# Performance work log

Hardware: AMD Instinct MI355X
Metric: run time of the kernel (lower is better)

The kernel has to match this reference:

```python
import jax, jax.numpy as jnp
import numpy as np

DIM = 1024
TOPK = 64
PAIRS = DIM // 2  # phase_pairs default
PHASE_MIX = 0.5
GATE_THRESHOLD = 0.0
EPS = 1e-12  # F.normalize default eps


def _l2norm(v):
    # matches F.normalize(v, dim=-1): v / max(||v||, eps)
    n = jnp.linalg.norm(v, axis=-1, keepdims=True)
    return v / jnp.maximum(n, EPS)


def setup_inputs() -> dict:
    key = jax.random.key(0)
    ks = jax.random.split(key, 6)
    s = 0.02  # small init scale for weights
    return {
        "x": jax.random.normal(ks[0], (4, 4096, DIM), dtype=jnp.float32),
        "gate_W": jax.random.normal(ks[1], (DIM, DIM), dtype=jnp.float32) * s,
        "gate_b": jnp.zeros((DIM,), dtype=jnp.float32),
        "mag_W": jax.random.normal(ks[2], (DIM, DIM), dtype=jnp.float32) * s,
        "mag_b": jnp.zeros((DIM,), dtype=jnp.float32),
        "Wq": jax.random.normal(ks[3], (DIM, DIM), dtype=jnp.float32) * s,
        "Wk": jax.random.normal(ks[4], (DIM, DIM), dtype=jnp.float32) * s,
        "phase_W": jax.random.normal(ks[5], (2 * PAIRS, DIM), dtype=jnp.float32) * s,
    }


def reference(x, gate_W, gate_b, mag_W, mag_b, Wq, Wk, phase_W):
    B, S, D = x.shape
    # gated SAE-style projection (gated=True, diag=False)
    gate_pre = x @ gate_W.T + gate_b          # [B,S,D]
    mag_pre = x @ mag_W.T + mag_b             # [B,S,D]
    # hard gate with straight-through estimator
    gate_soft = jax.nn.sigmoid(gate_pre)
    gate_hard = (gate_pre > GATE_THRESHOLD).astype(x.dtype)
    gate = gate_hard + gate_soft - jax.lax.stop_gradient(gate_soft)
    mag = jax.nn.relu(mag_pre)
    # top-k scatter mask along feature dim
    idx = jax.lax.top_k(gate_pre, TOPK)[1]    # [B,S,K]
    rows = jnp.arange(B * S)[:, None]
    mask = (jnp.zeros((B * S, D), dtype=bool)
            .at[rows, idx.reshape(B * S, TOPK)].set(True)
            .reshape(B, S, D))
    gate = jnp.where(mask, gate, jnp.zeros_like(gate))
    mag = jnp.where(mask, mag, jnp.zeros_like(mag))
    xg = gate * mag
    # twist projections, L2-normalized
    q = _l2norm(xg @ Wq.T)
    k = _l2norm(xg @ Wk.T)
    # symplectic momentum map over consecutive steps
    momentum_map = q[:, 1:] * k[:, :-1] - q[:, :-1] * k[:, 1:]  # [B,S-1,D]
    twist_mag = jnp.linalg.norm(momentum_map, axis=-1, keepdims=True)
    complexity = jnp.pad(jnp.tanh(twist_mag), ((0, 0), (1, 0), (0, 0)))  # [B,S,1]
    # phase branch (phase_mix > 0)
    phase = (xg @ phase_W.T).reshape(B, S, PAIRS, 2)
    phase = _l2norm(phase)
    pp, pc = phase[:, :-1], phase[:, 1:]
    cross = pp[..., 0] * pc[..., 1] - pp[..., 1] * pc[..., 0]   # [B,S-1,P]
    dot = jnp.clip(jnp.sum(pp * pc, axis=-1), -1.0, 1.0)
    phase_delta = jnp.abs(jnp.arctan2(cross, dot)) / jnp.pi
    phase_score = jnp.pad(jnp.mean(phase_delta, axis=-1, keepdims=True),
                          ((0, 0), (1, 0), (0, 0)))             # [B,S,1]
    return (1.0 - PHASE_MIX) * complexity + PHASE_MIX * phase_score
```

## Files before the change

kernel.cpp:

```cpp
#include <hip/hip_runtime.h>
#include <math.h>

#define DIM 1024
#define ROWS 16384
#define SEQ 4096
#define MARGIN 0.012f
#define MAXC 24

typedef __bf16 v8bf __attribute__((ext_vector_type(8)));
typedef float v4f __attribute__((ext_vector_type(4)));
typedef int v8i __attribute__((ext_vector_type(8)));

__device__ __forceinline__ unsigned short f2bf(float f){
  unsigned u = __float_as_uint(f);
  u = u + 0x7FFFu + ((u >> 16) & 1u);
  return (unsigned short)(u >> 16);
}
__device__ __forceinline__ float bf2f(unsigned short h){
  return __uint_as_float(((unsigned)h) << 16);
}
__device__ __forceinline__ unsigned short relu_bf(unsigned short h){
  return (h & 0x8000u) ? (unsigned short)0 : h;
}
__device__ __forceinline__ unsigned f2fp8(float f){
  float a = fabsf(f);
  unsigned sign = (__float_as_uint(f) >> 24) & 0x80u;
  if (a >= 448.f) return sign | 0x7Eu;
  if (a < 0.015625f){
    int k = (int)rintf(a * 512.f);
    if (k >= 8) return sign | 0x08u;
    return sign | (unsigned)k;
  }
  unsigned u = __float_as_uint(a);
  u += 0x7FFFFu + ((u >> 20) & 1u);
  int e = (int)((u >> 23) & 0xFFu) - 127;
  unsigned m = (u >> 20) & 7u;
  if (e > 8) return sign | 0x7Eu;
  return sign | ((unsigned)(e + 7) << 3) | m;
}
__device__ __forceinline__ void lds_fence(){
  __asm__ volatile("s_waitcnt lgkmcnt(0)" ::: "memory");
}

__global__ __launch_bounds__(256) void cvt_all(
    const float* __restrict__ x,
    const float* __restrict__ w0, const float* __restrict__ w1,
    const float* __restrict__ w2, const float* __restrict__ w3,
    const float* __restrict__ w4,
    unsigned short* __restrict__ xbf, unsigned short* __restrict__ wbf,
    unsigned char* __restrict__ wf8){
  const int y = blockIdx.y;
  int i = (blockIdx.x * 256 + threadIdx.x) * 4;
  if (y < 16){
    const float* s = x + ((size_t)y << 20);
    float4 f = *(const float4*)(s + i);
    ushort4 o; o.x = f2bf(f.x); o.y = f2bf(f.y); o.z = f2bf(f.z); o.w = f2bf(f.w);
    *(ushort4*)(xbf + ((size_t)y << 20) + i) = o;
  } else if (y < 18){
    const float* s = (y == 16) ? w0 : w1;
    float4 f = *(const float4*)(s + i);
    ushort4 o; o.x = f2bf(f.x); o.y = f2bf(f.y); o.z = f2bf(f.z); o.w = f2bf(f.w);
    *(ushort4*)(wbf + ((size_t)(y - 16) << 20) + i) = o;
  } else {
    const float* s = (y == 18) ? w2 : ((y == 19) ? w3 : w4);
    float4 f = *(const float4*)(s + i);
    unsigned u = f2fp8(f.x * 32.f) | (f2fp8(f.y * 32.f) << 8) |
                 (f2fp8(f.z * 32.f) << 16) | (f2fp8(f.w * 32.f) << 24);
    *(unsigned*)(wf8 + ((size_t)(y - 18) << 20) + i) = u;
  }
}

#define GBAR() asm volatile("s_barrier" ::: "memory")
#define GLGKM0() { asm volatile("s_waitcnt lgkmcnt(0)" ::: "memory"); __builtin_amdgcn_sched_barrier(0); }
#define GVM4() asm volatile("s_waitcnt vmcnt(4)" ::: "memory")
#define GVM8() asm volatile("s_waitcnt vmcnt(8)" ::: "memory")

__global__ __launch_bounds__(512, 2) void gemm_bt(
    const unsigned short* __restrict__ A, const unsigned short* __restrict__ B,
    const float* __restrict__ bias0, const float* __restrict__ bias1,
    unsigned short* __restrict__ C0, unsigned short* __restrict__ C1)
{
  extern __shared__ unsigned char lds[];
  const int t = threadIdx.x;
  const int lane = t & 63, wave = t >> 6;
  const int wr = wave >> 2, wc = wave & 3;
  const int bid = blockIdx.x;
  const int swz = (bid & 7) * 64 + (bid >> 3);
  const int m0 = (swz & 63) * 256;
  const int n0 = (swz >> 6) * 256;

  int offv[4];
#pragma unroll
  for (int h = 0; h < 2; h++)
#pragma unroll
    for (int i = 0; i < 2; i++){
      int o = h * 16384 + i * 8192 + t * 16;
      int u = o ^ (((o >> 9) & 1) << 5);
      int r = ((u >> 11) << 4) | ((u >> 6) & 15);
      int c = (((u >> 10) & 1) << 5) | ((u & 63) >> 1);
      offv[h * 2 + i] = r * 1024 + c;
    }
  const int off00 = offv[0], off01 = offv[1], off10 = offv[2], off11 = offv[3];
  const unsigned short* Ab = A + ((size_t)m0 << 10);
  const unsigned short* Bb = B + ((size_t)n0 << 10);

  const int laneterm = (lane & 15) * 64 + (((lane >> 4) * 16) ^ (((lane >> 3) & 1) * 32));
  const int aBase = wr * 16384 + laneterm;
  const int bBase = 32768 + wc * 8192 + laneterm;

#define GLD1(srcp, dsto) __builtin_amdgcn_global_load_lds( \
    (const __attribute__((address_space(1))) void*)(srcp), \
    (__attribute__((address_space(3))) void*)(lds + (dsto)), 16, 0, 0)

  auto stageA = [&](int h, int kt, int pp){
    const int o0 = h ? off10 : off00, o1 = h ? off11 : off01;
    GLD1(Ab + o0 + kt * 64, pp * 65536 + h * 16384 + t * 16);
    GLD1(Ab + o1 + kt * 64, pp * 65536 + h * 16384 + 8192 + t * 16);
  };
  auto stageB = [&](int h, int kt, int pp){
    const int o0 = h ? off10 : off00, o1 = h ? off11 : off01;
    GLD1(Bb + o0 + kt * 64, pp * 65536 + 32768 + h * 16384 + t * 16);
    GLD1(Bb + o1 + kt * 64, pp * 65536 + 32768 + h * 16384 + 8192 + t * 16);
  };

  v4f acc[8][4];
#pragma unroll
  for (int i = 0; i < 8; i++)
#pragma unroll
    for (int j = 0; j < 4; j++) acc[i][j] = v4f{0.f, 0.f, 0.f, 0.f};

  stageB(0, 0, 0); stageB(1, 0, 0);
  stageA(0, 0, 0); stageA(1, 0, 0);
  stageB(0, 1, 1); stageB(1, 1, 1);
  GVM4();
  GBAR();

  int p = 0;
  for (int X = 0; X < 16; X++, p ^= 1){
    const int pb = p * 65536;
    const int ktA = (X + 1 < 16) ? X + 1 : 15;
    const int ktB = (X + 2 < 16) ? X + 2 : X;
    v8bf a0[8], a1[8], b0[4], b1[4];

#pragma unroll
    for (int mi = 0; mi < 8; mi++) a0[mi] = *(const v8bf*)(lds + pb + aBase + mi * 2048);
#pragma unroll
    for (int ni = 0; ni < 4; ni++) b0[ni] = *(const v8bf*)(lds + pb + bBase + ni * 2048);
    stageA(0, ktA, p ^ 1);
    GBAR();
    __builtin_amdgcn_s_setprio(1);
#pragma unroll
    for (int mi = 0; mi < 4; mi++)
#pragma unroll
      for (int ni = 0; ni < 4; ni++)
        acc[mi][ni] = __builtin_amdgcn_mfma_f32_16x16x32_bf16(a0[mi], b0[ni], acc[mi][ni], 0, 0, 0);
    __builtin_amdgcn_s_setprio(0);
    GBAR();

#pragma unroll
    for (int mi = 0; mi < 4; mi++) a1[mi] = *(const v8bf*)(lds + pb + aBase + 1024 + mi * 2048);
#pragma unroll
    for (int ni = 0; ni < 4; ni++) b1[ni] = *(const v8bf*)(lds + pb + bBase + 1024 + ni * 2048);
    stageA(1, ktA, p ^ 1);
    GBAR();
    __builtin_amdgcn_s_setprio(1);
#pragma unroll
    for (int mi = 0; mi < 4; mi++)
#pragma unroll
      for (int ni = 0; ni < 4; ni++)
        acc[4 + mi][ni] = __builtin_amdgcn_mfma_f32_16x16x32_bf16(a0[4 + mi], b0[ni], acc[4 + mi][ni], 0, 0, 0);
    __builtin_amdgcn_s_setprio(0);
    GLGKM0();
    GBAR();

#pragma unroll
    for (int mi = 4; mi < 8; mi++) a1[mi] = *(const v8bf*)(lds + pb + aBase + 1024 + mi * 2048);
    stageB(0, ktB, p);
    GBAR();
    __builtin_amdgcn_s_setprio(1);
#pragma unroll
    for (int mi = 0; mi < 4; mi++)
#pragma unroll
      for (int ni = 0; ni < 4; ni++)
        acc[mi][ni] = __builtin_amdgcn_mfma_f32_16x16x32_bf16(a1[mi], b1[ni], acc[mi][ni], 0, 0, 0);
    __builtin_amdgcn_s_setprio(0);
    GBAR();

    stageB(1, ktB, p);
    GBAR();
    __builtin_amdgcn_s_setprio(1);
#pragma unroll
    for (int mi = 0; mi < 4; mi++)
#pragma unroll
      for (int ni = 0; ni < 4; ni++)
        acc[4 + mi][ni] = __builtin_amdgcn_mfma_f32_16x16x32_bf16(a1[4 + mi], b1[ni], acc[4 + mi][ni], 0, 0, 0);
    __builtin_amdgcn_s_setprio(0);
    GVM4();
    GBAR();
  }

  asm volatile("s_waitcnt vmcnt(0)" ::: "memory");
  __syncthreads();

  const int os = n0 >> 10;
  unsigned short* Cp = (os == 0) ? C0 : C1;
  const float* bp = (os == 0) ? bias0 : bias1;
  const int colbase = n0 & (DIM - 1);
  unsigned short* lt = (unsigned short*)lds;
  const int ar = lane & 15, aq = lane >> 4;
  const int lrw = wr * 16 + aq * 4;
  const int lrow = t >> 4;
  const int cseg = (t & 15) * 16;
  const size_t grb = (size_t)(m0 + (lrow >> 4) * 128 + (lrow & 15)) * DIM + colbase + cseg;
  float bv[4];
#pragma unroll
  for (int ni = 0; ni < 4; ni++) bv[ni] = bp[colbase + wc * 64 + ni * 16 + ar];
#pragma unroll
  for (int mi = 0; mi < 8; mi++){
#pragma unroll
    for (int ni = 0; ni < 4; ni++){
      const int colc = wc * 64 + ni * 16 + ar;
#pragma unroll
      for (int rr = 0; rr < 4; rr++)
        lt[(lrw + rr) * 264 + colc] = f2bf(acc[mi][ni][rr] + bv[ni]);
    }
    __syncthreads();
    uint4 v0 = *(const uint4*)&lt[lrow * 264 + cseg];
    uint4 v1 = *(const uint4*)&lt[lrow * 264 + cseg + 8];
    *(uint4*)(Cp + grb + (size_t)mi * 16 * DIM) = v0;
    *(uint4*)(Cp + grb + (size_t)mi * 16 * DIM + 8) = v1;
    __syncthreads();
  }
  asm volatile("s_waitcnt vmcnt(0)" ::: "memory");
}

__global__ __launch_bounds__(256, 2) void gemm8(
    const unsigned char* __restrict__ A, const unsigned char* __restrict__ B,
    unsigned short* __restrict__ C0, unsigned short* __restrict__ C1,
    unsigned short* __restrict__ C2)
{
  extern __shared__ unsigned char lds[];
  const int t = threadIdx.x;
  const int lane = t & 63, wave = t >> 6;
  const int wm = (wave >> 1) * 64;
  const int wn = (wave & 1) * 64;
  const int ar = lane & 15, aq = lane >> 4;

  const int bid = blockIdx.x;
  const int loc = bid >> 3;
  const int m0 = ((bid & 7) * 16 + (loc & 15)) * 128;
  const int n0 = (loc >> 4) * 128;

  const unsigned char* Ab = A + ((size_t)m0 << 10);
  const unsigned char* Bb = B + ((size_t)n0 << 10);

  int offb[4];
#pragma unroll
  for (int i = 0; i < 4; i++){
    int d = i * 4096 + t * 16;
    int row = d >> 7;
    offb[i] = row * 1024 + ((d & 127) ^ ((row & 7) << 4));
  }
  auto stage = [&](int kt, int p){
#pragma unroll
    for (int i = 0; i < 4; i++)
      GLD1(Ab + offb[i] + kt * 128, p * 32768 + i * 4096 + t * 16);
#pragma unroll
    for (int i = 0; i < 4; i++)
      GLD1(Bb + offb[i] + kt * 128, p * 32768 + 16384 + i * 4096 + t * 16);
  };
  auto rdfrag = [&](int boff, int r) -> v8i {
    int base = boff + r * 128 + ((aq * 32) ^ ((r & 7) << 4));
    int4 lo = *(const int4*)(lds + base);
    int4 hi = *(const int4*)(lds + (base ^ 16));
    v8i v; v[0]=lo.x; v[1]=lo.y; v[2]=lo.z; v[3]=lo.w;
           v[4]=hi.x; v[5]=hi.y; v[6]=hi.z; v[7]=hi.w;
    return v;
  };

  v4f acc[4][4];
#pragma unroll
  for (int i = 0; i < 4; i++)
#pragma unroll
    for (int j = 0; j < 4; j++) acc[i][j] = v4f{0.f, 0.f, 0.f, 0.f};

  stage(0, 0); stage(1, 1);
  GVM8();
  GBAR();

  for (int X = 0; X < 8; X++){
    const int p = X & 1, pb = p * 32768;
    v8i af[4], bf[4];
#pragma unroll
    for (int mi = 0; mi < 4; mi++) af[mi] = rdfrag(pb, wm + mi * 16 + ar);
#pragma unroll
    for (int ni = 0; ni < 4; ni++) bf[ni] = rdfrag(pb + 16384, wn + ni * 16 + ar);
    GLGKM0();
    GBAR();
    const int kt2 = (X + 2 < 8) ? X + 2 : X;
    stage(kt2, p);
    __builtin_amdgcn_s_setprio(1);
#pragma unroll
    for (int mi = 0; mi < 4; mi++)
#pragma unroll
      for (int ni = 0; ni < 4; ni++)
        acc[mi][ni] = __builtin_amdgcn_mfma_scale_f32_16x16x128_f8f6f4(
            af[mi], bf[ni], acc[mi][ni], 0, 0, 0, 127u, 0, 127u);
    __builtin_amdgcn_s_setprio(0);
    GVM8();
    GBAR();
  }

  asm volatile("s_waitcnt vmcnt(0)" ::: "memory");
  __syncthreads();
  const int os = n0 >> 10;
  unsigned short* Cp = (os == 0) ? C0 : ((os == 1) ? C1 : C2);
  const int colbase = n0 & (DIM - 1);
  unsigned short* lt = (unsigned short*)lds;
  const int lrw = (wave >> 1) * 16 + aq * 4;
  const int colc0 = (wave & 1) * 64;
  const int lrow = t >> 3;
  const int cseg = (t & 7) * 16;
  const size_t grb = (size_t)(m0 + (lrow >> 4) * 64 + (lrow & 15)) * DIM + colbase + cseg;
#pragma unroll
  for (int mi = 0; mi < 4; mi++){
#pragma unroll
    for (int ni = 0; ni < 4; ni++){
      const int colc = colc0 + ni * 16 + ar;
#pragma unroll
      for (int rr = 0; rr < 4; rr++)
        lt[(lrw + rr) * 136 + colc] = f2bf(acc[mi][ni][rr] * 0.03125f);
    }
    __syncthreads();
    uint4 v0 = *(const uint4*)&lt[lrow * 136 + cseg];
    uint4 v1 = *(const uint4*)&lt[lrow * 136 + cseg + 8];
    *(uint4*)(Cp + grb + (size_t)mi * 16 * DIM) = v0;
    *(uint4*)(Cp + grb + (size_t)mi * 16 * DIM + 8) = v1;
    __syncthreads();
  }
}

__global__ __launch_bounds__(256) void select_k(
  const unsigned short* __restrict__ gate_pre, const unsigned short* __restrict__ mag_pre,
  const float* __restrict__ x, const float* __restrict__ gW, const float* __restrict__ gb,
  unsigned char* __restrict__ xg8)
{
  __shared__ int   s_h  [4][256];
  __shared__ int   s_cnt[4];
  __shared__ int   s_idx[4][MAXC];
  __shared__ float s_ex [4][MAXC];
  __shared__ int   s_res[4][MAXC];

  const int t = threadIdx.x;
  const int lane = t & 63, wave = t >> 6;
  const int row = blockIdx.x * 4 + wave;
  const size_t rb = (size_t)row * DIM;

  uint4 ga = *(const uint4*)(gate_pre + rb + lane * 8);
  uint4 gB = *(const uint4*)(gate_pre + rb + 512 + lane * 8);
  float4 xa0 = *(const float4*)(x + rb + lane * 8);
  float4 xa1 = *(const float4*)(x + rb + lane * 8 + 4);
  float4 xb0 = *(const float4*)(x + rb + 512 + lane * 8);
  float4 xb1 = *(const float4*)(x + rb + 512 + lane * 8 + 4);
  uint4 ma = *(const uint4*)(mag_pre + rb + lane * 8);
  uint4 mb = *(const uint4*)(mag_pre + rb + 512 + lane * 8);

  unsigned gw[8] = {ga.x, ga.y, ga.z, ga.w, gB.x, gB.y, gB.z, gB.w};
  unsigned mw[8] = {ma.x, ma.y, ma.z, ma.w, mb.x, mb.y, mb.z, mb.w};
  float vg[16], vm[16];
  unsigned kk[16];
#pragma unroll
  for (int j = 0; j < 8; j++){
    unsigned w = gw[j];
    vg[2*j]   = __uint_as_float(w << 16);
    vg[2*j+1] = __uint_as_float(w & 0xFFFF0000u);
    unsigned lo = w & 0xFFFFu, hi = w >> 16;
    kk[2*j]   = (lo & 0x8000u) ? (~lo & 0xFFFFu) : (lo | 0x8000u);
    kk[2*j+1] = (hi & 0x8000u) ? (~hi & 0xFFFFu) : (hi | 0x8000u);
    unsigned m = mw[j];
    vm[2*j]   = __uint_as_float(m << 16);
    vm[2*j+1] = __uint_as_float(m & 0xFFFF0000u);
  }
  float vx[16] = {xa0.x, xa0.y, xa0.z, xa0.w, xa1.x, xa1.y, xa1.z, xa1.w,
                  xb0.x, xb0.y, xb0.z, xb0.w, xb1.x, xb1.y, xb1.z, xb1.w};

  if (lane == 0) s_cnt[wave] = 0;

  auto findbin = [&](int rk, int &bout, int &Cout){
    int c0 = s_h[wave][lane*4+0], c1 = s_h[wave][lane*4+1];
    int c2 = s_h[wave][lane*4+2], c3 = s_h[wave][lane*4+3];
    int sl = c0 + c1 + c2 + c3;
    int tt = sl;
#pragma unroll
    for (int m = 1; m < 64; m <<= 1){
      int u = __shfl(tt, lane + m);
      if (lane + m < 64) tt += u;
    }
    int ab = tt - sl;
    int bb = -1, CC = 0;
    int a3 = ab;       if (a3 < rk && rk <= a3 + c3){ bb = lane*4+3; CC = a3; }
    int a2 = ab + c3;  if (bb < 0 && a2 < rk && rk <= a2 + c2){ bb = lane*4+2; CC = a2; }
    int a1 = a2 + c2;  if (bb < 0 && a1 < rk && rk <= a1 + c1){ bb = lane*4+1; CC = a1; }
    int a0 = a1 + c1;  if (bb < 0 && a0 < rk && rk <= a0 + c0){ bb = lane*4+0; CC = a0; }
    unsigned long long mk = __ballot(bb >= 0);
    int src = (int)__ffsll(mk) - 1;
    bout = __shfl(bb, src); Cout = __shfl(CC, src);
  };

  s_h[wave][lane*4+0] = 0; s_h[wave][lane*4+1] = 0;
  s_h[wave][lane*4+2] = 0; s_h[wave][lane*4+3] = 0;
  lds_fence();
#pragma unroll
  for (int e = 0; e < 16; e++) atomicAdd(&s_h[wave][kk[e] >> 8], 1);
  lds_fence();
  int b1, C1; findbin(64, b1, C1);

  s_h[wave][lane*4+0] = 0; s_h[wave][lane*4+1] = 0;
  s_h[wave][lane*4+2] = 0; s_h[wave][lane*4+3] = 0;
  lds_fence();
#pragma unroll
  for (int e = 0; e < 16; e++)
    if ((int)(kk[e] >> 8) == b1) atomicAdd(&s_h[wave][kk[e] & 255u], 1);
  lds_fence();
  int b2, C2; findbin(64 - C1, b2, C2);

  unsigned tkey = ((unsigned)b1 << 8) | (unsigned)b2;
  unsigned hthr = (tkey & 0x8000u) ? (tkey & 0x7FFFu) : (~tkey & 0xFFFFu);
  const float thr = bf2f((unsigned short)hthr);
  const float cl = thr - MARGIN, ch = thr + MARGIN;

  int n1 = 0;
#pragma unroll
  for (int e = 0; e < 16; e++) n1 += (vg[e] > ch) ? 1 : 0;
#pragma unroll
  for (int m = 32; m; m >>= 1) n1 += __shfl_xor(n1, m);
  const int s = 64 - n1;

  lds_fence();
#pragma unroll
  for (int e = 0; e < 16; e++){
    float vv = vg[e];
    if (vv >= cl && vv <= ch){
      int p = atomicAdd(&s_cnt[wave], 1);
      if (p < MAXC) s_idx[wave][p] = (e >> 3) * 512 + lane * 8 + (e & 7);
    }
  }
  lds_fence();
  int namb = s_cnt[wave]; if (namb > MAXC) namb = MAXC;

  const int o0 = lane * 8, o1 = lane * 8 + 4, o2 = 512 + lane * 8, o3 = 512 + lane * 8 + 4;
  float4 w0, w1, w2, w3;
  int dcur = 0;
  if (namb > 0){
    dcur = s_idx[wave][0];
    const float* wr0 = gW + (size_t)dcur * DIM;
    w0 = *(const float4*)(wr0 + o0); w1 = *(const float4*)(wr0 + o1);
    w2 = *(const float4*)(wr0 + o2); w3 = *(const float4*)(wr0 + o3);
  }
  for (int i = 0; i < namb; i++){
    float4 c0 = w0, c1 = w1, c2 = w2, c3 = w3;
    int dn = 0;
    if (i + 1 < namb){
      dn = s_idx[wave][i + 1];
      const float* wr2 = gW + (size_t)dn * DIM;
      w0 = *(const float4*)(wr2 + o0); w1 = *(const float4*)(wr2 + o1);
      w2 = *(const float4*)(wr2 + o2); w3 = *(const float4*)(wr2 + o3);
    }
    float p = 0.f;
    p = fmaf(vx[0], c0.x, p);  p = fmaf(vx[1], c0.y, p);
    p = fmaf(vx[2], c0.z, p);  p = fmaf(vx[3], c0.w, p);
    p = fmaf(vx[4], c1.x, p);  p = fmaf(vx[5], c1.y, p);
    p = fmaf(vx[6], c1.z, p);  p = fmaf(vx[7], c1.w, p);
    p = fmaf(vx[8], c2.x, p);  p = fmaf(vx[9], c2.y, p);
    p = fmaf(vx[10], c2.z, p); p = fmaf(vx[11], c2.w, p);
    p = fmaf(vx[12], c3.x, p); p = fmaf(vx[13], c3.y, p);
    p = fmaf(vx[14], c3.z, p); p = fmaf(vx[15], c3.w, p);
#pragma unroll
    for (int m = 32; m; m >>= 1) p += __shfl_xor(p, m);
    if (lane == 0) s_ex[wave][i] = p + gb[dcur];
    dcur = dn;
  }
  lds_fence();

  if (lane < namb){
    float e = s_ex[wave][lane]; int d = s_idx[wave][lane];
    int rank = 0;
    for (int j = 0; j < namb; j++){
      float ej = s_ex[wave][j]; int dj = s_idx[wave][j];
      if (ej > e || (ej == e && dj < d)) rank++;
    }
    s_res[wave][lane] = (rank < s && e > 0.f) ? 1 : 0;
  }
  lds_fence();

  unsigned inb = 0, rsm = 0;
  for (int i = 0; i < namb; i++){
    int d = s_idx[wave][i];
    if (((d & 511) >> 3) == lane){
      int e = (d >> 9) * 8 + (d & 7);
      inb |= 1u << e;
      if (s_res[wave][i]) rsm |= 1u << e;
    }
  }

  float vals[16];
#pragma unroll
  for (int e = 0; e < 16; e++){
    float mv = (vm[e] > 0.f) ? vm[e] : 0.f;
    float v = (vg[e] > ch && vg[e] > 0.f) ? mv : 0.f;
    if ((inb >> e) & 1u) v = ((rsm >> e) & 1u) ? mv : 0.f;
    vals[e] = v;
  }

  unsigned pk[4];
#pragma unroll
  for (int q = 0; q < 4; q++){
    unsigned a = 0, b = 0;
    asm volatile("v_cvt_pk_fp8_f32 %0, %1, %2" : "+v"(a) : "v"(vals[4*q+0]), "v"(vals[4*q+1]));
    asm volatile("v_cvt_pk_fp8_f32 %0, %1, %2" : "+v"(b) : "v"(vals[4*q+2]), "v"(vals[4*q+3]));
    pk[q] = (a & 0xFFFFu) | (b << 16);
  }
  uint2 st0; st0.x = pk[0]; st0.y = pk[1];
  uint2 st1; st1.x = pk[2]; st1.y = pk[3];
  *(uint2*)(xg8 + rb + lane * 8) = st0;
  *(uint2*)(xg8 + rb + 512 + lane * 8) = st1;
}

__global__ __launch_bounds__(256) void epilogue_k(
  const unsigned short* __restrict__ q_pre, const unsigned short* __restrict__ k_pre,
  const unsigned short* __restrict__ p_pre, float* __restrict__ out)
{
  const int r0 = blockIdx.x * 4;
  const int t = threadIdx.x;
  const int lane = t & 63, wave = t >> 6;
  __shared__ float red[16];

  const int rp = (r0 == 0) ? 0 : r0 - 1;
  float vqp[4], vkp[4], vpp[4];
  {
    ushort4 uq = *(const ushort4*)(q_pre + (size_t)rp * DIM + 4*t);
    ushort4 uk = *(const ushort4*)(k_pre + (size_t)rp * DIM + 4*t);
    ushort4 up = *(const ushort4*)(p_pre + (size_t)rp * DIM + 4*t);
    vqp[0]=bf2f(uq.x); vqp[1]=bf2f(uq.y); vqp[2]=bf2f(uq.z); vqp[3]=bf2f(uq.w);
    vkp[0]=bf2f(uk.x); vkp[1]=bf2f(uk.y); vkp[2]=bf2f(uk.z); vkp[3]=bf2f(uk.w);
    vpp[0]=bf2f(up.x); vpp[1]=bf2f(up.y); vpp[2]=bf2f(up.z); vpp[3]=bf2f(up.w);
  }
  float aq = 0.f, ak = 0.f;
#pragma unroll
  for (int j = 0; j < 4; j++){ aq = fmaf(vqp[j], vqp[j], aq); ak = fmaf(vkp[j], vkp[j], ak); }
#pragma unroll
  for (int m = 32; m; m >>= 1){ aq += __shfl_xor(aq, m); ak += __shfl_xor(ak, m); }
  if (lane == 0){ red[wave] = aq; red[4 + wave] = ak; }
  __syncthreads();
  float rqp = 1.f / fmaxf(sqrtf(red[0] + red[1] + red[2] + red[3]), 1e-12f);
  float rkp = 1.f / fmaxf(sqrtf(red[4] + red[5] + red[6] + red[7]), 1e-12f);
  __syncthreads();

  for (int rr = 0; rr < 4; rr++){
    const int r = r0 + rr;
    float vqc[4], vkc[4], vpc[4];
    {
      ushort4 uq = *(const ushort4*)(q_pre + (size_t)r * DIM + 4*t);
      ushort4 uk = *(const ushort4*)(k_pre + (size_t)r * DIM + 4*t);
      ushort4 up = *(const ushort4*)(p_pre + (size_t)r * DIM + 4*t);
      vqc[0]=bf2f(uq.x); vqc[1]=bf2f(uq.y); vqc[2]=bf2f(uq.z); vqc[3]=bf2f(uq.w);
      vkc[0]=bf2f(uk.x); vkc[1]=bf2f(uk.y); vkc[2]=bf2f(uk.z); vkc[3]=bf2f(uk.w);
      vpc[0]=bf2f(up.x); vpc[1]=bf2f(up.y); vpc[2]=bf2f(up.z); vpc[3]=bf2f(up.w);
    }
    const bool seg = (r & (SEQ - 1)) == 0;
    float aqc = 0.f, akc = 0.f;
#pragma unroll
    for (int j = 0; j < 4; j++){ aqc = fmaf(vqc[j], vqc[j], aqc); akc = fmaf(vkc[j], vkc[j], akc); }
    float dsum = 0.f;
    if (!seg){
#pragma unroll
      for (int j = 0; j < 2; j++){
        float ax = vpp[2*j], ay = vpp[2*j+1], bx = vpc[2*j], by = vpc[2*j+1];
        float ia = 1.f / fmaxf(sqrtf(ax * ax + ay * ay), 1e-12f);
        float ib = 1.f / fmaxf(sqrtf(bx * bx + by * by), 1e-12f);
        ax *= ia; ay *= ia; bx *= ib; by *= ib;
        float cross = ax * by - ay * bx;
        float dot = fminf(fmaxf(ax * bx + ay * by, -1.f), 1.f);
        dsum += fabsf(atan2f(cross, dot)) * 0.3183098861837907f;
      }
    }
#pragma unroll
    for (int m = 32; m; m >>= 1){
      aqc += __shfl_xor(aqc, m); akc += __shfl_xor(akc, m); dsum += __shfl_xor(dsum, m);
    }
    if (lane == 0){ red[wave] = aqc; red[4 + wave] = akc; red[8 + wave] = dsum; }
    __syncthreads();
    float rqc = 1.f / fmaxf(sqrtf(red[0] + red[1] + red[2] + red[3]), 1e-12f);
    float rkc = 1.f / fmaxf(sqrtf(red[4] + red[5] + red[6] + red[7]), 1e-12f);
    if (!seg){
      float tw = 0.f;
#pragma unroll
      for (int j = 0; j < 4; j++){
        float m = (vqc[j] * rqc) * (vkp[j] * rkp) - (vqp[j] * rqp) * (vkc[j] * rkc);
        tw = fmaf(m, m, tw);
      }
#pragma unroll
      for (int m = 32; m; m >>= 1) tw += __shfl_xor(tw, m);
      if (lane == 0) red[12 + wave] = tw;
      __syncthreads();
      if (t == 0){
        float dtot = red[8] + red[9] + red[10] + red[11];
        float twt = red[12] + red[13] + red[14] + red[15];
        out[r] = 0.5f * tanhf(sqrtf(twt)) + 0.5f * (dtot * (1.f / 512.f));
      }
    } else {
      if (t == 0) out[r] = 0.f;
    }
    __syncthreads();
#pragma unroll
    for (int j = 0; j < 4; j++){ vqp[j] = vqc[j]; vkp[j] = vkc[j]; vpp[j] = vpc[j]; }
    rqp = rqc; rkp = rkc;
  }
}

extern "C" void kernel_launch(void* const* d_in, const int* in_sizes, int n_in,
                              void* d_out, int out_size, void* d_ws, size_t ws_size,
                              hipStream_t stream)
{
  const float* x       = (const float*)d_in[0];
  const float* gate_W  = (const float*)d_in[1];
  const float* gate_b  = (const float*)d_in[2];
  const float* mag_W   = (const float*)d_in[3];
  const float* mag_b   = (const float*)d_in[4];
  const float* Wq      = (const float*)d_in[5];
  const float* Wk      = (const float*)d_in[6];
  const float* phase_W = (const float*)d_in[7];
  float* out = (float*)d_out;

  char* ws = (char*)d_ws;
  unsigned short* xbf = (unsigned short*)ws;
  unsigned short* wbf = (unsigned short*)(ws + 33554432);
  unsigned char*  wf8 = (unsigned char*)(ws + 37748736);
  unsigned short* gate_pre = (unsigned short*)(ws + 41943040);
  unsigned short* mag_pre  = (unsigned short*)(ws + 75497472);
  unsigned short* p_pre    = (unsigned short*)(ws + 109051904);
  unsigned short* q_pre = gate_pre;
  unsigned short* k_pre = mag_pre;

  static bool attr_set = false;
  if (!attr_set){
    hipFuncSetAttribute((const void*)gemm_bt,
                        hipFuncAttributeMaxDynamicSharedMemorySize, 131072);
    hipFuncSetAttribute((const void*)gemm8,
                        hipFuncAttributeMaxDynamicSharedMemorySize, 65536);
    attr_set = true;
  }

  dim3 b256(256);
  cvt_all<<<dim3(1024, 21), b256, 0, stream>>>(x, gate_W, mag_W, Wq, Wk, phase_W,
                                               xbf, wbf, wf8);

  gemm_bt<<<dim3(512), dim3(512), 131072, stream>>>(xbf, wbf, gate_b, mag_b,
                                                    gate_pre, mag_pre);

  unsigned char* xg8 = (unsigned char*)xbf;
  select_k<<<ROWS / 4, b256, 0, stream>>>(gate_pre, mag_pre, x, gate_W, gate_b, xg8);

  gemm8<<<dim3(3072), b256, 65536, stream>>>(xg8, wf8, q_pre, k_pre, p_pre);

  epilogue_k<<<ROWS / 4, b256, 0, stream>>>(q_pre, k_pre, p_pre, out);
}
```

Measured before the change: 366.5 us.

## Switch bf16 gate/mag GEMM to 128x128 tiles with simpler double-buffered pipeline

Replaces the 256x256-tile, 512-thread bf16 GEMM, which used a four-phase interleaved load/MFMA schedule, with 128x128 tiles on 256 threads. Each K step now loads 128-wide K slices through an XOR-swizzled LDS layout, and each iteration reads all fragments at once before a single barrier. The aim is more blocks (2048 instead of 512) and fewer barriers per iteration, so the GPU's CUs are better filled and the sync overhead drops. In exchange, each output tile reuses its loaded data less, so global and L2 traffic per FLOP goes up, and less load latency is hidden behind MFMA work.

Result: slower. 381.4 us (+4.1%).

```diff
diff --git a/kernel.cpp b/kernel.cpp
--- a/kernel.cpp
+++ b/kernel.cpp
@@ -72,10 +72,13 @@
 
 #define GBAR() asm volatile("s_barrier" ::: "memory")
 #define GLGKM0() { asm volatile("s_waitcnt lgkmcnt(0)" ::: "memory"); __builtin_amdgcn_sched_barrier(0); }
-#define GVM4() asm volatile("s_waitcnt vmcnt(4)" ::: "memory")
 #define GVM8() asm volatile("s_waitcnt vmcnt(8)" ::: "memory")
 
-__global__ __launch_bounds__(512, 2) void gemm_bt(
+#define GLD1(srcp, dsto) __builtin_amdgcn_global_load_lds( \
+    (const __attribute__((address_space(1))) void*)(srcp), \
+    (__attribute__((address_space(3))) void*)(lds + (dsto)), 16, 0, 0)
+
+__global__ __launch_bounds__(256, 2) void gemm_bt(
     const unsigned short* __restrict__ A, const unsigned short* __restrict__ B,
     const float* __restrict__ bias0, const float* __restrict__ bias1,
     unsigned short* __restrict__ C0, unsigned short* __restrict__ C1)
@@ -83,155 +86,112 @@
   extern __shared__ unsigned char lds[];
   const int t = threadIdx.x;
   const int lane = t & 63, wave = t >> 6;
-  const int wr = wave >> 2, wc = wave & 3;
+  const int wm = (wave >> 1) * 64;
+  const int wn = (wave & 1) * 64;
+  const int ar = lane & 15, aq = lane >> 4;
+
   const int bid = blockIdx.x;
-  const int swz = (bid & 7) * 64 + (bid >> 3);
-  const int m0 = (swz & 63) * 256;
-  const int n0 = (swz >> 6) * 256;
-
-  int offv[4];
-#pragma unroll
-  for (int h = 0; h < 2; h++)
-#pragma unroll
-    for (int i = 0; i < 2; i++){
-      int o = h * 16384 + i * 8192 + t * 16;
-      int u = o ^ (((o >> 9) & 1) << 5);
-      int r = ((u >> 11) << 4) | ((u >> 6) & 15);
-      int c = (((u >> 10) & 1) << 5) | ((u & 63) >> 1);
-      offv[h * 2 + i] = r * 1024 + c;
-    }
-  const int off00 = offv[0], off01 = offv[1], off10 = offv[2], off11 = offv[3];
-  const unsigned short* Ab = A + ((size_t)m0 << 10);
-  const unsigned short* Bb = B + ((size_t)n0 << 10);
-
-  const int laneterm = (lane & 15) * 64 + (((lane >> 4) * 16) ^ (((lane >> 3) & 1) * 32));
-  const int aBase = wr * 16384 + laneterm;
-  const int bBase = 32768 + wc * 8192 + laneterm;
-
-#define GLD1(srcp, dsto) __builtin_amdgcn_global_load_lds( \
-    (const __attribute__((address_space(1))) void*)(srcp), \
-    (__attribute__((address_space(3))) void*)(lds + (dsto)), 16, 0, 0)
-
-  auto stageA = [&](int h, int kt, int pp){
-    const int o0 = h ? off10 : off00, o1 = h ? off11 : off01;
-    GLD1(Ab + o0 + kt * 64, pp * 65536 + h * 16384 + t * 16);
-    GLD1(Ab + o1 + kt * 64, pp * 65536 + h * 16384 + 8192 + t * 16);
+  const int loc = bid >> 3;
+  const int m0 = ((bid & 7) * 16 + (loc & 15)) * 128;
+  const int n0 = (loc >> 4) * 128;
+
+  const unsigned char* Ab = (const unsigned char*)A + (size_t)m0 * 2048;
+  const unsigned char* Bb = (const unsigned char*)B + (size_t)n0 * 2048;
+
+  int offb[4];
+#pragma unroll
+  for (int i = 0; i < 4; i++){
+    int d = i * 4096 + t * 16;
+    int row = d >> 7;
+    offb[i] = row * 2048 + ((d & 127) ^ ((row & 7) << 4));
+  }
+  auto stage = [&](int kt, int p){
+#pragma unroll
+    for (int i = 0; i < 4; i++)
+      GLD1(Ab + offb[i] + kt * 128, p * 32768 + i * 4096 + t * 16);
+#pragma unroll
+    for (int i = 0; i < 4; i++)
+      GLD1(Bb + offb[i] + kt * 128, p * 32768 + 16384 + i * 4096 + t * 16);
   };
-  auto stageB = [&](int h, int kt, int pp){
-    const int o0 = h ? off10 : off00, o1 = h ? off11 : off01;
-    GLD1(Bb + o0 + kt * 64, pp * 65536 + 32768 + h * 16384 + t * 16);
-    GLD1(Bb + o1 + kt * 64, pp * 65536 + 32768 + h * 16384 + 8192 + t * 16);
+  auto rdf = [&](int boff, int r, int h) -> v8bf {
+    int base = boff + r * 128 + ((h * 64 + aq * 16) ^ ((r & 7) << 4));
+    return *(const v8bf*)(lds + base);
   };
 
-  v4f acc[8][4];
-#pragma unroll
-  for (int i = 0; i < 8; i++)
+  v4f acc[4][4];
+#pragma unroll
+  for (int i = 0; i < 4; i++)
 #pragma unroll
     for (int j = 0; j < 4; j++) acc[i][j] = v4f{0.f, 0.f, 0.f, 0.f};
 
-  stageB(0, 0, 0); stageB(1, 0, 0);
-  stageA(0, 0, 0); stageA(1, 0, 0);
-  stageB(0, 1, 1); stageB(1, 1, 1);
-  GVM4();
+  stage(0, 0); stage(1, 1);
+  GVM8();
   GBAR();
 
-  int p = 0;
-  for (int X = 0; X < 16; X++, p ^= 1){
-    const int pb = p * 65536;
-    const int ktA = (X + 1 < 16) ? X + 1 : 15;
-    const int ktB = (X + 2 < 16) ? X + 2 : X;
-    v8bf a0[8], a1[8], b0[4], b1[4];
-
-#pragma unroll
-    for (int mi = 0; mi < 8; mi++) a0[mi] = *(const v8bf*)(lds + pb + aBase + mi * 2048);
-#pragma unroll
-    for (int ni = 0; ni < 4; ni++) b0[ni] = *(const v8bf*)(lds + pb + bBase + ni * 2048);
-    stageA(0, ktA, p ^ 1);
-    GBAR();
-    __builtin_amdgcn_s_setprio(1);
-#pragma unroll
-    for (int mi = 0; mi < 4; mi++)
-#pragma unroll
-      for (int ni = 0; ni < 4; ni++)
-        acc[mi][ni] = __builtin_amdgcn_mfma_f32_16x16x32_bf16(a0[mi], b0[ni], acc[mi][ni], 0, 0, 0);
-    __builtin_amdgcn_s_setprio(0);
-    GBAR();
-
-#pragma unroll
-    for (int mi = 0; mi < 4; mi++) a1[mi] = *(const v8bf*)(lds + pb + aBase + 1024 + mi * 2048);
-#pragma unroll
-    for (int ni = 0; ni < 4; ni++) b1[ni] = *(const v8bf*)(lds + pb + bBase + 1024 + ni * 2048);
-    stageA(1, ktA, p ^ 1);
-    GBAR();
-    __builtin_amdgcn_s_setprio(1);
-#pragma unroll
-    for (int mi = 0; mi < 4; mi++)
-#pragma unroll
-      for (int ni = 0; ni < 4; ni++)
-        acc[4 + mi][ni] = __builtin_amdgcn_mfma_f32_16x16x32_bf16(a0[4 + mi], b0[ni], acc[4 + mi][ni], 0, 0, 0);
-    __builtin_amdgcn_s_setprio(0);
+  for (int X = 0; X < 16; X++){
+    const int p = X & 1, pb = p * 32768;
+    v8bf af0[4], af1[4], bf0[4], bf1[4];
+#pragma unroll
+    for (int mi = 0; mi < 4; mi++){
+      af0[mi] = rdf(pb, wm + mi * 16 + ar, 0);
+      af1[mi] = rdf(pb, wm + mi * 16 + ar, 1);
+    }
+#pragma unroll
+    for (int ni = 0; ni < 4; ni++){
+      bf0[ni] = rdf(pb + 16384, wn + ni * 16 + ar, 0);
+      bf1[ni] = rdf(pb + 16384, wn + ni * 16 + ar, 1);
+    }
     GLGKM0();
     GBAR();
-
-#pragma unroll
-    for (int mi = 4; mi < 8; mi++) a1[mi] = *(const v8bf*)(lds + pb + aBase + 1024 + mi * 2048);
-    stageB(0, ktB, p);
-    GBAR();
+    const int kt2 = (X + 2 < 16) ? X + 2 : X;
+    stage(kt2, p);
     __builtin_amdgcn_s_setprio(1);
 #pragma unroll
     for (int mi = 0; mi < 4; mi++)
 #pragma unroll
       for (int ni = 0; ni < 4; ni++)
-        acc[mi][ni] = __builtin_amdgcn_mfma_f32_16x16x32_bf16(a1[mi], b1[ni], acc[mi][ni], 0, 0, 0);
+        acc[mi][ni] = __builtin_amdgcn_mfma_f32_16x16x32_bf16(af0[mi], bf0[ni], acc[mi][ni], 0, 0, 0);
+#pragma unroll
+    for (int mi = 0; mi < 4; mi++)
+#pragma unroll
+      for (int ni = 0; ni < 4; ni++)
+        acc[mi][ni] = __builtin_amdgcn_mfma_f32_16x16x32_bf16(af1[mi], bf1[ni], acc[mi][ni], 0, 0, 0);
     __builtin_amdgcn_s_setprio(0);
-    GBAR();
-
-    stageB(1, ktB, p);
-    GBAR();
-    __builtin_amdgcn_s_setprio(1);
-#pragma unroll
-    for (int mi = 0; mi < 4; mi++)
-#pragma unroll
-      for (int ni = 0; ni < 4; ni++)
-        acc[4 + mi][ni] = __builtin_amdgcn_mfma_f32_16x16x32_bf16(a1[4 + mi], b1[ni], acc[4 + mi][ni], 0, 0, 0);
-    __builtin_amdgcn_s_setprio(0);
-    GVM4();
+    GVM8();
     GBAR();
   }
 
   asm volatile("s_waitcnt vmcnt(0)" ::: "memory");
   __syncthreads();
-
   const int os = n0 >> 10;
   unsigned short* Cp = (os == 0) ? C0 : C1;
   const float* bp = (os == 0) ? bias0 : bias1;
   const int colbase = n0 & (DIM - 1);
   unsigned short* lt = (unsigned short*)lds;
-  const int ar = lane & 15, aq = lane >> 4;
-  const int lrw = wr * 16 + aq * 4;
-  const int lrow = t >> 4;
-  const int cseg = (t & 15) * 16;
-  const size_t grb = (size_t)(m0 + (lrow >> 4) * 128 + (lrow & 15)) * DIM + colbase + cseg;
+  const int lrw = (wave >> 1) * 16 + aq * 4;
+  const int colc0 = (wave & 1) * 64;
   float bv[4];
 #pragma unroll
-  for (int ni = 0; ni < 4; ni++) bv[ni] = bp[colbase + wc * 64 + ni * 16 + ar];
-#pragma unroll
-  for (int mi = 0; mi < 8; mi++){
+  for (int ni = 0; ni < 4; ni++) bv[ni] = bp[colbase + colc0 + ni * 16 + ar];
+  const int lrow = t >> 3;
+  const int cseg = (t & 7) * 16;
+  const size_t grb = (size_t)(m0 + (lrow >> 4) * 64 + (lrow & 15)) * DIM + colbase + cseg;
+#pragma unroll
+  for (int mi = 0; mi < 4; mi++){
 #pragma unroll
     for (int ni = 0; ni < 4; ni++){
-      const int colc = wc * 64 + ni * 16 + ar;
+      const int colc = colc0 + ni * 16 + ar;
 #pragma unroll
       for (int rr = 0; rr < 4; rr++)
-        lt[(lrw + rr) * 264 + colc] = f2bf(acc[mi][ni][rr] + bv[ni]);
+        lt[(lrw + rr) * 136 + colc] = f2bf(acc[mi][ni][rr] + bv[ni]);
     }
     __syncthreads();
-    uint4 v0 = *(const uint4*)&lt[lrow * 264 + cseg];
-    uint4 v1 = *(const uint4*)&lt[lrow * 264 + cseg + 8];
+    uint4 v0 = *(const uint4*)&lt[lrow * 136 + cseg];
+    uint4 v1 = *(const uint4*)&lt[lrow * 136 + cseg + 8];
     *(uint4*)(Cp + grb + (size_t)mi * 16 * DIM) = v0;
     *(uint4*)(Cp + grb + (size_t)mi * 16 * DIM + 8) = v1;
     __syncthreads();
   }
-  asm volatile("s_waitcnt vmcnt(0)" ::: "memory");
 }
 
 __global__ __launch_bounds__(256, 2) void gemm8(
@@ -645,7 +605,7 @@
   static bool attr_set = false;
   if (!attr_set){
     hipFuncSetAttribute((const void*)gemm_bt,
-                        hipFuncAttributeMaxDynamicSharedMemorySize, 131072);
+                        hipFuncAttributeMaxDynamicSharedMemorySize, 65536);
     hipFuncSetAttribute((const void*)gemm8,
                         hipFuncAttributeMaxDynamicSharedMemorySize, 65536);
     attr_set = true;
@@ -655,8 +615,8 @@
   cvt_all<<<dim3(1024, 21), b256, 0, stream>>>(x, gate_W, mag_W, Wq, Wk, phase_W,
                                                xbf, wbf, wf8);
 
-  gemm_bt<<<dim3(512), dim3(512), 131072, stream>>>(xbf, wbf, gate_b, mag_b,
-                                                    gate_pre, mag_pre);
+  gemm_bt<<<dim3(2048), b256, 65536, stream>>>(xbf, wbf, gate_b, mag_b,
+                                               gate_pre, mag_pre);
 
   unsigned char* xg8 = (unsigned char*)xbf;
   select_k<<<ROWS / 4, b256, 0, stream>>>(gate_pre, mag_pre, x, gate_W, gate_b, xg8);
```
